# Kernel tuning notes

Measured on AMD Instinct MI355X. Metric: run time of the kernel, lower is better.

The kernel has to match this reference:

```python
import jax, jax.numpy as jnp
import numpy as np

B, C, H, W = 16, 512, 32, 32
NUM_HEADS = 8
GROUPS = 32
EPS = 1e-5


def setup_inputs() -> dict:
    key = jax.random.key(0)
    ks = jax.random.split(key, 3)
    x = jax.random.normal(ks[0], (B, C, H, W), dtype=jnp.float32)
    # Conv2d 1x1 weights stored as (out, in); init ~ fan-in scaled normal
    qkv_w = jax.random.normal(ks[1], (3 * C, C), dtype=jnp.float32) * (C ** -0.5)
    proj_w = jax.random.normal(ks[2], (C, C), dtype=jnp.float32) * (C ** -0.5)
    return {
        "x": x,
        "norm_w": jnp.ones((C,), jnp.float32),
        "norm_b": jnp.zeros((C,), jnp.float32),
        "qkv_w": qkv_w,
        "qkv_b": jnp.zeros((3 * C,), jnp.float32),
        "proj_w": proj_w,
        "proj_b": jnp.zeros((C,), jnp.float32),
    }


def reference(x, norm_w, norm_b, qkv_w, qkv_b, proj_w, proj_b):
    b, c, hh, ww = x.shape
    nh = NUM_HEADS
    hd = c // nh
    n = hh * ww

    # GroupNorm(32, C)
    xg = x.reshape(b, GROUPS, c // GROUPS, hh, ww)
    mean = xg.mean(axis=(2, 3, 4), keepdims=True)
    var = ((xg - mean) ** 2).mean(axis=(2, 3, 4), keepdims=True)
    hn = ((xg - mean) * jax.lax.rsqrt(var + EPS)).reshape(b, c, hh, ww)
    hn = hn * norm_w[None, :, None, None] + norm_b[None, :, None, None]

    # 1x1 conv QKV projection
    qkv = jnp.einsum('bchw,oc->bohw', hn, qkv_w) + qkv_b[None, :, None, None]
    # (B,3C,H,W) -> (B,3,nh,hd,N) -> (3,B,nh,N,hd)
    qkv = qkv.reshape(b, 3, nh, hd, n).transpose(1, 0, 2, 4, 3)
    q, k, v = qkv[0], qkv[1], qkv[2]

    scale = hd ** -0.5
    attn = jax.nn.softmax(jnp.einsum('bhnd,bhmd->bhnm', q, k) * scale, axis=-1)
    o = jnp.einsum('bhnm,bhmd->bhnd', attn, v)  # (B,nh,N,hd)
    o = o.transpose(0, 1, 3, 2).reshape(b, c, hh, ww)

    out = jnp.einsum('bchw,oc->bohw', o, proj_w) + proj_b[None, :, None, None]
    return out + x
```

## Files before the change

kernel.cpp:

```cpp
#include <hip/hip_runtime.h>
#include <cstdint>
#include <math.h>


typedef __bf16 bf16;
typedef __attribute__((ext_vector_type(8))) __bf16 bf16x8;
typedef __attribute__((ext_vector_type(4))) float f32x4;
typedef __attribute__((ext_vector_type(4))) short s16x4;

union U8 { uint4 u4; bf16x8 v; bf16 h[8]; };
union U4 { ushort4 u; bf16 h[4]; };
union UB4 { ushort4 u; s16x4 s; bf16 h[4]; };
union F4 { float4 v; float f[4]; };

typedef __attribute__((address_space(1))) void* gp1;
typedef __attribute__((address_space(3))) void* lp3;

__device__ __forceinline__ void async16(const void* g, void* l) {
  __builtin_amdgcn_global_load_lds((gp1)g, (lp3)l, 16, 0, 0);
}

#define LOG2E 1.44269504f

__global__ __launch_bounds__(256) void cvt_w(const float* __restrict__ qw,
                                             const float* __restrict__ pw,
                                             bf16* __restrict__ qwb,
                                             bf16* __restrict__ pwb) {
  int i = blockIdx.x * 256 + threadIdx.x;
  F4 v; bf16* dst;
  if (i < 196608) { v.v = ((const float4*)qw)[i]; dst = qwb + (size_t)i * 4; }
  else { v.v = ((const float4*)pw)[i - 196608]; dst = pwb + (size_t)(i - 196608) * 4; }
  U4 o;
#pragma unroll
  for (int j = 0; j < 4; j++) o.h[j] = (bf16)v.f[j];
  *(ushort4*)dst = o.u;
}

__global__ __launch_bounds__(256) void gn_stats(const float* __restrict__ x,
                                                float2* __restrict__ stats) {
  int bg = blockIdx.x;
  const float* base = x + (size_t)bg * 16384;
  int t = threadIdx.x;
  float s = 0.f, ss = 0.f;
#pragma unroll
  for (int p = 0; p < 16; p++) {
    F4 u; u.v = *(const float4*)(base + (size_t)(p * 256 + t) * 4);
#pragma unroll
    for (int i = 0; i < 4; i++) { float v = u.f[i]; s += v; ss += v * v; }
  }
  for (int off = 1; off < 64; off <<= 1) { s += __shfl_xor(s, off); ss += __shfl_xor(ss, off); }
  __shared__ float red[8];
  int w = t >> 6;
  if ((t & 63) == 0) { red[w] = s; red[4 + w] = ss; }
  __syncthreads();
  if (t == 0) {
    float S = red[0] + red[1] + red[2] + red[3];
    float SS = red[4] + red[5] + red[6] + red[7];
    float mean = S * (1.f / 16384.f);
    float var = SS * (1.f / 16384.f) - mean * mean;
    stats[bg] = make_float2(mean, rsqrtf(var + 1e-5f));
  }
}

__global__ __launch_bounds__(256) void gn_apply(const float* __restrict__ x,
                                                const float* __restrict__ nwp,
                                                const float* __restrict__ nbp,
                                                const float2* __restrict__ stats,
                                                bf16* __restrict__ hnt) {
  int b = blockIdx.z, nt = blockIdx.y, ct = blockIdx.x;
  int t = threadIdx.x, w = t >> 6, l = t & 63;
  int wc = w & 1, wn = w >> 1;
  int cb = ct * 128 + wc * 64 + (l & 7) * 8;
  int n0 = nt * 64 + wn * 32 + (l >> 3) * 4;
  float2 ms = stats[b * 32 + (cb >> 4)];
  float wgt[8], bia[8];
#pragma unroll
  for (int i = 0; i < 8; i++) {
    float wi = nwp[cb + i] * ms.y;
    wgt[i] = wi;
    bia[i] = nbp[cb + i] - ms.x * wi;
  }
  F4 in[8];
  const float* xb = x + ((size_t)b * 512 + cb) * 1024 + n0;
#pragma unroll
  for (int i = 0; i < 8; i++) in[i].v = *(const float4*)(xb + (size_t)i * 1024);
  bf16* ob = hnt + ((size_t)b * 1024 + n0) * 512 + cb;
#pragma unroll
  for (int j = 0; j < 4; j++) {
    U8 o;
#pragma unroll
    for (int i = 0; i < 8; i++) o.h[i] = (bf16)(in[i].f[j] * wgt[i] + bia[i]);
    *(uint4*)(ob + (size_t)j * 512) = o.u4;
  }
}

__device__ __forceinline__ void gemm_bt_core(const bf16* ga0, const bf16* gb0,
                                             bf16* At, bf16* Bt,
                                             f32x4 (&acc)[4][4], int w, int l) {
  const bf16* ga = ga0 + (size_t)(w * 16 + (l >> 2)) * 512 + (l & 3) * 8;
  const bf16* gb = gb0 + (size_t)(w * 16 + (l >> 2)) * 512 + (l & 3) * 8;
  int wr = w >> 1, wc = w & 1;
  const bf16* Ab = At + (wr * 64 + (l & 15)) * 32 + (l >> 4) * 8;
  const bf16* Bb = Bt + (wc * 64 + (l & 15)) * 32 + (l >> 4) * 8;
  bf16* lA = At + w * 16 * 32;
  bf16* lB = Bt + w * 16 * 32;
  for (int k0 = 0; k0 < 512; k0 += 32) {
    async16(ga + k0, lA);
    async16(ga + 64 * 512 + k0, lA + 64 * 32);
    async16(gb + k0, lB);
    async16(gb + 64 * 512 + k0, lB + 64 * 32);
    __syncthreads();
    bf16x8 af[4], bfr[4];
#pragma unroll
    for (int i = 0; i < 4; i++) {
      af[i] = *(const bf16x8*)(Ab + i * 512);
      bfr[i] = *(const bf16x8*)(Bb + i * 512);
    }
#pragma unroll
    for (int i = 0; i < 4; i++)
#pragma unroll
      for (int j = 0; j < 4; j++)
        acc[i][j] = __builtin_amdgcn_mfma_f32_16x16x32_bf16(af[i], bfr[j], acc[i][j], 0, 0, 0);
    __syncthreads();
  }
}

__global__ __launch_bounds__(256, 2) void qkv_gemm(const bf16* __restrict__ hnt,
                                                   const bf16* __restrict__ qwb,
                                                   const float* __restrict__ qb,
                                                   bf16* __restrict__ qsw,
                                                   bf16* __restrict__ ksw,
                                                   bf16* __restrict__ vsw) {
  __shared__ bf16 At[128 * 32];
  __shared__ bf16 Bt[128 * 32];
  int b = blockIdx.z, mt = blockIdx.y, ot = blockIdx.x;
  int m0 = mt * 128, o0 = ot * 128;
  int t = threadIdx.x, w = t >> 6, l = t & 63;
  f32x4 acc[4][4] = {};
  gemm_bt_core(hnt + ((size_t)b * 1024 + m0) * 512, qwb + (size_t)o0 * 512, At, Bt, acc, w, l);

  int wr = w >> 1, wc = w & 1, quad = l >> 4, li = l & 15;
#pragma unroll
  for (int i = 0; i < 4; i++) {
    int gnb = m0 + wr * 64 + i * 16;
    int blk = gnb >> 4;
#pragma unroll
    for (int j = 0; j < 4; j++) {
      int go = o0 + wc * 64 + j * 16 + li;
      float bias = qb[go];
      if (ot < 8) {
        int c = (ot < 4) ? go : (go - 512);
        int hh = c >> 6, d = c & 63;
        int ks = d >> 5, dq = (d >> 3) & 3, jj = d & 7;
        bf16* base = ((ot < 4) ? qsw : ksw) + ((size_t)(b * 8 + hh) << 16)
                     + (blk * 2 + ks) * 512 + dq * 8 + jj;
#pragma unroll
        for (int r = 0; r < 4; r++)
          base[(quad * 4 + r) * 32] = (bf16)(acc[i][j][r] + bias);
      } else {
        int c = go - 1024;
        int hh = c >> 6, d = c & 63;
        int df = d >> 4, lv = d & 15;
        bf16* base = vsw + ((size_t)(b * 8 + hh) << 16)
                     + (blk * 4 + df) * 256 + (lv * 4 + quad) * 4;
        U4 pk;
#pragma unroll
        for (int r = 0; r < 4; r++) pk.h[r] = (bf16)(acc[i][j][r] + bias);
        *(ushort4*)base = pk.u;
      }
    }
  }
}

__global__ __launch_bounds__(256, 4) void attn(const bf16* __restrict__ qsw,
                                               const bf16* __restrict__ ksw,
                                               const bf16* __restrict__ vsw,
                                               bf16* __restrict__ ont) {
  int bh = blockIdx.x;
  int b = bh >> 3, h = bh & 7;
  int qt = blockIdx.y;
  int t = threadIdx.x, w = t >> 6, l = t & 63;
  int quad = l >> 4, li = l & 15;
  int q0 = qt * 128 + w * 32;

  int laneK = (li * 4 + quad) * 8;
  int laneV = (li * 4 + quad) * 4;
  const bf16* qp = qsw + ((size_t)bh << 16) + laneK;
  const bf16* kp = ksw + ((size_t)bh << 16) + laneK;
  const bf16* vp = vsw + ((size_t)bh << 16) + laneV;

  const float QS = 0.125f * LOG2E;
  bf16x8 qfr[2][2];
#pragma unroll
  for (int qf = 0; qf < 2; qf++)
#pragma unroll
    for (int ks = 0; ks < 2; ks++) {
      U8 u;
      u.u4 = *(const uint4*)(qp + (((q0 >> 4) + qf) * 2 + ks) * 512);
#pragma unroll
      for (int i = 0; i < 8; i++) u.h[i] = (bf16)((float)u.h[i] * QS);
      qfr[qf][ks] = u.v;
    }

  float mrun[2] = {-INFINITY, -INFINITY}, lrun[2] = {0.f, 0.f};
  f32x4 of[4][2] = {};

  U8 ka[2], kc[2];
#pragma unroll
  for (int kf = 0; kf < 2; kf++) {
    ka[kf].u4 = *(const uint4*)(kp + kf * 1024);
    kc[kf].u4 = *(const uint4*)(kp + kf * 1024 + 512);
  }

  for (int c = 0; c < 32; c++) {
    int cb = c * 2048;
    UB4 va[2][4];
#pragma unroll
    for (int kf = 0; kf < 2; kf++)
#pragma unroll
      for (int df = 0; df < 4; df++)
        va[kf][df].u = *(const ushort4*)(vp + cb + kf * 1024 + df * 256);
    f32x4 st[2][2] = {};
#pragma unroll
    for (int kf = 0; kf < 2; kf++) {
      st[0][kf] = __builtin_amdgcn_mfma_f32_16x16x32_bf16(ka[kf].v, qfr[0][0], st[0][kf], 0, 0, 0);
      st[1][kf] = __builtin_amdgcn_mfma_f32_16x16x32_bf16(ka[kf].v, qfr[1][0], st[1][kf], 0, 0, 0);
      st[0][kf] = __builtin_amdgcn_mfma_f32_16x16x32_bf16(kc[kf].v, qfr[0][1], st[0][kf], 0, 0, 0);
      st[1][kf] = __builtin_amdgcn_mfma_f32_16x16x32_bf16(kc[kf].v, qfr[1][1], st[1][kf], 0, 0, 0);
    }
    int cn = ((c + 1) & 31) * 2048;
    U8 nka[2], nkc[2];
#pragma unroll
    for (int kf = 0; kf < 2; kf++) {
      nka[kf].u4 = *(const uint4*)(kp + cn + kf * 1024);
      nkc[kf].u4 = *(const uint4*)(kp + cn + kf * 1024 + 512);
    }
    UB4 pfr[2][2];
#pragma unroll
    for (int qf = 0; qf < 2; qf++) {
      f32x4 vm = st[qf][0];
#pragma unroll
      for (int r = 0; r < 4; r++) vm[r] = fmaxf(vm[r], st[qf][1][r]);
      float mt = fmaxf(fmaxf(vm[0], vm[1]), fmaxf(vm[2], vm[3]));
      mt = fmaxf(mt, __shfl_xor(mt, 16));
      mt = fmaxf(mt, __shfl_xor(mt, 32));
      float mold = mrun[qf];
      float mnew = fmaxf(mold, mt);
      mrun[qf] = mnew;
      f32x4 vs = {};
#pragma unroll
      for (int kf = 0; kf < 2; kf++)
#pragma unroll
        for (int r = 0; r < 4; r++) {
          float e = __builtin_amdgcn_exp2f(st[qf][kf][r] - mnew);
          vs[r] += e;
          pfr[qf][kf].h[r] = (bf16)e;
        }
      float ls = (vs[0] + vs[1]) + (vs[2] + vs[3]);
      ls += __shfl_xor(ls, 16);
      ls += __shfl_xor(ls, 32);
      if (__ballot(mnew > mold)) {
        float alpha = __builtin_amdgcn_exp2f(mold - mnew);
        lrun[qf] = lrun[qf] * alpha + ls;
#pragma unroll
        for (int df = 0; df < 4; df++)
#pragma unroll
          for (int r = 0; r < 4; r++) of[df][qf][r] *= alpha;
      } else {
        lrun[qf] += ls;
      }
    }
#pragma unroll
    for (int kf = 0; kf < 2; kf++)
#pragma unroll
      for (int df = 0; df < 4; df++)
#pragma unroll
        for (int qf = 0; qf < 2; qf++)
          of[df][qf] = __builtin_amdgcn_mfma_f32_16x16x16bf16_1k(va[kf][df].s, pfr[qf][kf].s, of[df][qf], 0, 0, 0);
#pragma unroll
    for (int kf = 0; kf < 2; kf++) { ka[kf] = nka[kf]; kc[kf] = nkc[kf]; }
  }
#pragma unroll
  for (int qf = 0; qf < 2; qf++) {
    float inv = 1.f / lrun[qf];
    bf16* ob = ont + ((size_t)b * 1024 + q0 + qf * 16 + li) * 512 + h * 64 + quad * 4;
#pragma unroll
    for (int df = 0; df < 4; df++) {
      U4 pk;
#pragma unroll
      for (int r = 0; r < 4; r++) pk.h[r] = (bf16)(of[df][qf][r] * inv);
      *(ushort4*)(ob + df * 16) = pk.u;
    }
  }
}

__global__ __launch_bounds__(256, 2) void proj_gemm(const bf16* __restrict__ ont,
                                                    const bf16* __restrict__ pwb,
                                                    const float* __restrict__ pb,
                                                    const float* __restrict__ x,
                                                    float* __restrict__ out) {
  __shared__ bf16 At[128 * 32];
  __shared__ bf16 Bt[128 * 32];
  int b = blockIdx.z, mt = blockIdx.y, ot = blockIdx.x;
  int m0 = mt * 128, o0 = ot * 128;
  int t = threadIdx.x, w = t >> 6, l = t & 63;
  f32x4 acc[4][4] = {};
  gemm_bt_core(ont + ((size_t)b * 1024 + m0) * 512, pwb + (size_t)o0 * 512, At, Bt, acc, w, l);

  int wr = w >> 1, wc = w & 1, quad = l >> 4, li = l & 15;
#pragma unroll
  for (int i = 0; i < 4; i++) {
    int gn = m0 + wr * 64 + i * 16 + quad * 4;
#pragma unroll
    for (int j = 0; j < 4; j++) {
      int go = o0 + wc * 64 + j * 16 + li;
      float bias = pb[go];
      F4 xres; xres.v = *(const float4*)(x + ((size_t)b * 512 + go) * 1024 + gn);
      F4 o;
#pragma unroll
      for (int r = 0; r < 4; r++) o.f[r] = acc[i][j][r] + bias + xres.f[r];
      *(float4*)(out + ((size_t)b * 512 + go) * 1024 + gn) = o.v;
    }
  }
}

extern "C" void kernel_launch(void* const* d_in, const int* in_sizes, int n_in,
                              void* d_out, int out_size, void* d_ws, size_t ws_size,
                              hipStream_t stream) {
  const float* x  = (const float*)d_in[0];
  const float* nw = (const float*)d_in[1];
  const float* nb = (const float*)d_in[2];
  const float* qw = (const float*)d_in[3];
  const float* qb = (const float*)d_in[4];
  const float* pw = (const float*)d_in[5];
  const float* pb = (const float*)d_in[6];
  float* out = (float*)d_out;

  char* ws = (char*)d_ws;
  float2* stats = (float2*)ws;
  bf16* qwb = (bf16*)(ws + (64u << 10));
  bf16* pwb = (bf16*)(ws + (2u << 20));
  bf16* hnt = (bf16*)(ws + (4u << 20));
  bf16* qsw = (bf16*)(ws + (20u << 20));
  bf16* ksw = (bf16*)(ws + (36u << 20));
  bf16* vsw = (bf16*)(ws + (52u << 20));
  bf16* ont = hnt;

  cvt_w<<<1024, 256, 0, stream>>>(qw, pw, qwb, pwb);
  gn_stats<<<512, 256, 0, stream>>>(x, stats);
  gn_apply<<<dim3(4, 16, 16), 256, 0, stream>>>(x, nw, nb, stats, hnt);
  qkv_gemm<<<dim3(12, 8, 16), 256, 0, stream>>>(hnt, qwb, qb, qsw, ksw, vsw);
  attn<<<dim3(128, 8, 1), 256, 0, stream>>>(qsw, ksw, vsw, ont);
  proj_gemm<<<dim3(4, 8, 16), 256, 0, stream>>>(ont, pwb, pb, x, out);
}
```

Before: 230.1 us.

## Replace online softmax with two-pass exact max then exp-sum attention

The attention kernel now makes a first pass over all keys computing QK^T only to find the exact row max, then a second pass recomputes QK^T, exponentiates against the fixed max, and accumulates PV and the row sum. This removes the per-chunk cross-lane max/sum shuffles, the ballot branch and the rescaling of the output accumulators. In exchange the QK^T MFMAs and K loads are doubled, and the register-prefetch of the next K chunk is dropped.

```diff
diff --git a/kernel.cpp b/kernel.cpp
--- a/kernel.cpp
+++ b/kernel.cpp
@@ -202,15 +202,41 @@
       qfr[qf][ks] = u.v;
     }
 
-  float mrun[2] = {-INFINITY, -INFINITY}, lrun[2] = {0.f, 0.f};
+  f32x4 vmax[2];
+#pragma unroll
+  for (int qf = 0; qf < 2; qf++) vmax[qf] = f32x4{-INFINITY, -INFINITY, -INFINITY, -INFINITY};
+
+  for (int c = 0; c < 32; c++) {
+    int cb = c * 2048;
+    f32x4 st[2][2] = {};
+#pragma unroll
+    for (int kf = 0; kf < 2; kf++) {
+      U8 ka, kc;
+      ka.u4 = *(const uint4*)(kp + cb + kf * 1024);
+      kc.u4 = *(const uint4*)(kp + cb + kf * 1024 + 512);
+      st[0][kf] = __builtin_amdgcn_mfma_f32_16x16x32_bf16(ka.v, qfr[0][0], st[0][kf], 0, 0, 0);
+      st[1][kf] = __builtin_amdgcn_mfma_f32_16x16x32_bf16(ka.v, qfr[1][0], st[1][kf], 0, 0, 0);
+      st[0][kf] = __builtin_amdgcn_mfma_f32_16x16x32_bf16(kc.v, qfr[0][1], st[0][kf], 0, 0, 0);
+      st[1][kf] = __builtin_amdgcn_mfma_f32_16x16x32_bf16(kc.v, qfr[1][1], st[1][kf], 0, 0, 0);
+    }
+#pragma unroll
+    for (int qf = 0; qf < 2; qf++)
+#pragma unroll
+      for (int kf = 0; kf < 2; kf++)
+#pragma unroll
+        for (int r = 0; r < 4; r++) vmax[qf][r] = fmaxf(vmax[qf][r], st[qf][kf][r]);
+  }
+  float m[2];
+#pragma unroll
+  for (int qf = 0; qf < 2; qf++) {
+    float mt = fmaxf(fmaxf(vmax[qf][0], vmax[qf][1]), fmaxf(vmax[qf][2], vmax[qf][3]));
+    mt = fmaxf(mt, __shfl_xor(mt, 16));
+    mt = fmaxf(mt, __shfl_xor(mt, 32));
+    m[qf] = mt;
+  }
+
+  f32x4 lacc[2] = {};
   f32x4 of[4][2] = {};
-
-  U8 ka[2], kc[2];
-#pragma unroll
-  for (int kf = 0; kf < 2; kf++) {
-    ka[kf].u4 = *(const uint4*)(kp + kf * 1024);
-    kc[kf].u4 = *(const uint4*)(kp + kf * 1024 + 512);
-  }
 
   for (int c = 0; c < 32; c++) {
     int cb = c * 2048;
@@ -223,53 +249,25 @@
     f32x4 st[2][2] = {};
 #pragma unroll
     for (int kf = 0; kf < 2; kf++) {
-      st[0][kf] = __builtin_amdgcn_mfma_f32_16x16x32_bf16(ka[kf].v, qfr[0][0], st[0][kf], 0, 0, 0);
-      st[1][kf] = __builtin_amdgcn_mfma_f32_16x16x32_bf16(ka[kf].v, qfr[1][0], st[1][kf], 0, 0, 0);
-      st[0][kf] = __builtin_amdgcn_mfma_f32_16x16x32_bf16(kc[kf].v, qfr[0][1], st[0][kf], 0, 0, 0);
-      st[1][kf] = __builtin_amdgcn_mfma_f32_16x16x32_bf16(kc[kf].v, qfr[1][1], st[1][kf], 0, 0, 0);
-    }
-    int cn = ((c + 1) & 31) * 2048;
-    U8 nka[2], nkc[2];
-#pragma unroll
-    for (int kf = 0; kf < 2; kf++) {
-      nka[kf].u4 = *(const uint4*)(kp + cn + kf * 1024);
-      nkc[kf].u4 = *(const uint4*)(kp + cn + kf * 1024 + 512);
+      U8 ka, kc;
+      ka.u4 = *(const uint4*)(kp + cb + kf * 1024);
+      kc.u4 = *(const uint4*)(kp + cb + kf * 1024 + 512);
+      st[0][kf] = __builtin_amdgcn_mfma_f32_16x16x32_bf16(ka.v, qfr[0][0], st[0][kf], 0, 0, 0);
+      st[1][kf] = __builtin_amdgcn_mfma_f32_16x16x32_bf16(ka.v, qfr[1][0], st[1][kf], 0, 0, 0);
+      st[0][kf] = __builtin_amdgcn_mfma_f32_16x16x32_bf16(kc.v, qfr[0][1], st[0][kf], 0, 0, 0);
+      st[1][kf] = __builtin_amdgcn_mfma_f32_16x16x32_bf16(kc.v, qfr[1][1], st[1][kf], 0, 0, 0);
     }
     UB4 pfr[2][2];
 #pragma unroll
-    for (int qf = 0; qf < 2; qf++) {
-      f32x4 vm = st[qf][0];
-#pragma unroll
-      for (int r = 0; r < 4; r++) vm[r] = fmaxf(vm[r], st[qf][1][r]);
-      float mt = fmaxf(fmaxf(vm[0], vm[1]), fmaxf(vm[2], vm[3]));
-      mt = fmaxf(mt, __shfl_xor(mt, 16));
-      mt = fmaxf(mt, __shfl_xor(mt, 32));
-      float mold = mrun[qf];
-      float mnew = fmaxf(mold, mt);
-      mrun[qf] = mnew;
-      f32x4 vs = {};
+    for (int qf = 0; qf < 2; qf++)
 #pragma unroll
       for (int kf = 0; kf < 2; kf++)
 #pragma unroll
         for (int r = 0; r < 4; r++) {
-          float e = __builtin_amdgcn_exp2f(st[qf][kf][r] - mnew);
-          vs[r] += e;
+          float e = __builtin_amdgcn_exp2f(st[qf][kf][r] - m[qf]);
+          lacc[qf][r] += e;
           pfr[qf][kf].h[r] = (bf16)e;
         }
-      float ls = (vs[0] + vs[1]) + (vs[2] + vs[3]);
-      ls += __shfl_xor(ls, 16);
-      ls += __shfl_xor(ls, 32);
-      if (__ballot(mnew > mold)) {
-        float alpha = __builtin_amdgcn_exp2f(mold - mnew);
-        lrun[qf] = lrun[qf] * alpha + ls;
-#pragma unroll
-        for (int df = 0; df < 4; df++)
-#pragma unroll
-          for (int r = 0; r < 4; r++) of[df][qf][r] *= alpha;
-      } else {
-        lrun[qf] += ls;
-      }
-    }
 #pragma unroll
     for (int kf = 0; kf < 2; kf++)
 #pragma unroll
@@ -277,12 +275,14 @@
 #pragma unroll
         for (int qf = 0; qf < 2; qf++)
           of[df][qf] = __builtin_amdgcn_mfma_f32_16x16x16bf16_1k(va[kf][df].s, pfr[qf][kf].s, of[df][qf], 0, 0, 0);
-#pragma unroll
-    for (int kf = 0; kf < 2; kf++) { ka[kf] = nka[kf]; kc[kf] = nkc[kf]; }
-  }
+  }
+
 #pragma unroll
   for (int qf = 0; qf < 2; qf++) {
-    float inv = 1.f / lrun[qf];
+    float ls = (lacc[qf][0] + lacc[qf][1]) + (lacc[qf][2] + lacc[qf][3]);
+    ls += __shfl_xor(ls, 16);
+    ls += __shfl_xor(ls, 32);
+    float inv = 1.f / ls;
     bf16* ob = ont + ((size_t)b * 1024 + q0 + qf * 16 + li) * 512 + h * 64 + quad * 4;
 #pragma unroll
     for (int df = 0; df < 4; df++) {
```

New measurement: 258.0 us. 1.12x slower.

## Stage K/V tiles through double-buffered LDS with async global loads

Applied to the files above, without the earlier changes.

Each attention block cooperatively loads every K and V chunk once into shared memory with global_load_lds async copies, double-buffered. Each wave then reads its MFMA fragments from LDS instead of every wave fetching the same K/V data from global memory into registers. This cuts redundant global/L2 traffic across the four waves and frees registers used for K prefetch. The cost is a block-wide barrier every iteration and LDS read latency on the critical path; correctness depends on the async copy being complete before the barrier is crossed.

```diff
diff --git a/kernel.cpp b/kernel.cpp
--- a/kernel.cpp
+++ b/kernel.cpp
@@ -176,6 +176,8 @@
                                                const bf16* __restrict__ ksw,
                                                const bf16* __restrict__ vsw,
                                                bf16* __restrict__ ont) {
+  __shared__ __align__(16) bf16 kld[2][2048];
+  __shared__ __align__(16) bf16 vld[2][2048];
   int bh = blockIdx.x;
   int b = bh >> 3, h = bh & 7;
   int qt = blockIdx.y;
@@ -186,8 +188,11 @@
   int laneK = (li * 4 + quad) * 8;
   int laneV = (li * 4 + quad) * 4;
   const bf16* qp = qsw + ((size_t)bh << 16) + laneK;
-  const bf16* kp = ksw + ((size_t)bh << 16) + laneK;
-  const bf16* vp = vsw + ((size_t)bh << 16) + laneV;
+  const bf16* kg = ksw + ((size_t)bh << 16) + l * 8;
+  const bf16* vg = vsw + ((size_t)bh << 16) + l * 8;
+
+  async16(kg + w * 512, &kld[0][w * 512]);
+  async16(vg + w * 512, &vld[0][w * 512]);
 
   const float QS = 0.125f * LOG2E;
   bf16x8 qfr[2][2];
@@ -205,36 +210,30 @@
   float mrun[2] = {-INFINITY, -INFINITY}, lrun[2] = {0.f, 0.f};
   f32x4 of[4][2] = {};
 
-  U8 ka[2], kc[2];
-#pragma unroll
-  for (int kf = 0; kf < 2; kf++) {
-    ka[kf].u4 = *(const uint4*)(kp + kf * 1024);
-    kc[kf].u4 = *(const uint4*)(kp + kf * 1024 + 512);
-  }
+  __syncthreads();
 
   for (int c = 0; c < 32; c++) {
-    int cb = c * 2048;
+    int buf = c & 1, nb = buf ^ 1;
+    int cn = ((c + 1) & 31) * 2048;
+    async16(kg + cn + w * 512, &kld[nb][w * 512]);
+    async16(vg + cn + w * 512, &vld[nb][w * 512]);
+    f32x4 st[2][2] = {};
+#pragma unroll
+    for (int kf = 0; kf < 2; kf++) {
+      U8 ka, kc;
+      ka.v = *(const bf16x8*)(&kld[buf][kf * 1024 + laneK]);
+      kc.v = *(const bf16x8*)(&kld[buf][kf * 1024 + 512 + laneK]);
+      st[0][kf] = __builtin_amdgcn_mfma_f32_16x16x32_bf16(ka.v, qfr[0][0], st[0][kf], 0, 0, 0);
+      st[1][kf] = __builtin_amdgcn_mfma_f32_16x16x32_bf16(ka.v, qfr[1][0], st[1][kf], 0, 0, 0);
+      st[0][kf] = __builtin_amdgcn_mfma_f32_16x16x32_bf16(kc.v, qfr[0][1], st[0][kf], 0, 0, 0);
+      st[1][kf] = __builtin_amdgcn_mfma_f32_16x16x32_bf16(kc.v, qfr[1][1], st[1][kf], 0, 0, 0);
+    }
     UB4 va[2][4];
 #pragma unroll
     for (int kf = 0; kf < 2; kf++)
 #pragma unroll
       for (int df = 0; df < 4; df++)
-        va[kf][df].u = *(const ushort4*)(vp + cb + kf * 1024 + df * 256);
-    f32x4 st[2][2] = {};
-#pragma unroll
-    for (int kf = 0; kf < 2; kf++) {
-      st[0][kf] = __builtin_amdgcn_mfma_f32_16x16x32_bf16(ka[kf].v, qfr[0][0], st[0][kf], 0, 0, 0);
-      st[1][kf] = __builtin_amdgcn_mfma_f32_16x16x32_bf16(ka[kf].v, qfr[1][0], st[1][kf], 0, 0, 0);
-      st[0][kf] = __builtin_amdgcn_mfma_f32_16x16x32_bf16(kc[kf].v, qfr[0][1], st[0][kf], 0, 0, 0);
-      st[1][kf] = __builtin_amdgcn_mfma_f32_16x16x32_bf16(kc[kf].v, qfr[1][1], st[1][kf], 0, 0, 0);
-    }
-    int cn = ((c + 1) & 31) * 2048;
-    U8 nka[2], nkc[2];
-#pragma unroll
-    for (int kf = 0; kf < 2; kf++) {
-      nka[kf].u4 = *(const uint4*)(kp + cn + kf * 1024);
-      nkc[kf].u4 = *(const uint4*)(kp + cn + kf * 1024 + 512);
-    }
+        va[kf][df].u = *(const ushort4*)(&vld[buf][kf * 1024 + df * 256 + laneV]);
     UB4 pfr[2][2];
 #pragma unroll
     for (int qf = 0; qf < 2; qf++) {
@@ -277,8 +276,7 @@
 #pragma unroll
         for (int qf = 0; qf < 2; qf++)
           of[df][qf] = __builtin_amdgcn_mfma_f32_16x16x16bf16_1k(va[kf][df].s, pfr[qf][kf].s, of[df][qf], 0, 0, 0);
-#pragma unroll
-    for (int kf = 0; kf < 2; kf++) { ka[kf] = nka[kf]; kc[kf] = nkc[kf]; }
+    __syncthreads();
   }
 #pragma unroll
   for (int qf = 0; qf < 2; qf++) {
```

Measured after the change: 235.4 us. 2.3% more time.
